# Performance work log

Hardware: AMD Instinct MI355X
Metric: run time of the kernel (lower is better)

## Reference

```python
import math
import jax, jax.numpy as jnp
import numpy as np

N_HEAD = 4
D_MODEL = 96
BS, N_TOK = 32, 512
A2LEN = 150          # a2len % 16 != 0 so padn > 0 (asserted in torch code)
DST_MXLEN = 32


def setup_inputs() -> dict:
    key = jax.random.key(0)
    k1, k2, k3, k4, k5, k6 = jax.random.split(key, 6)
    x = jax.random.normal(k1, (BS, N_TOK, D_MODEL), dtype=jnp.float32)
    # LinearM: w is [outdim, indim+1], last column is the bias, zeroed at init
    wqv_w = 0.02 * jax.random.normal(k2, (3 * D_MODEL, D_MODEL + 1), dtype=jnp.float32)
    wqv_w = wqv_w.at[:, -1].set(0.0)
    fanout_w = 0.02 * jax.random.normal(k3, (D_MODEL, D_MODEL + 1), dtype=jnp.float32)
    fanout_w = fanout_w.at[:, -1].set(0.0)

    def make_coo(k):
        # COO triples [dst, src, dst_cnt]; every dst has DST_MXLEN sources
        dst = jnp.repeat(jnp.arange(N_TOK), DST_MXLEN)
        src = jax.random.randint(k, (N_TOK * DST_MXLEN,), 0, N_TOK)
        cnt = jnp.tile(jnp.arange(DST_MXLEN), N_TOK)
        return jnp.stack([dst, src, cnt], axis=1).astype(jnp.int32)

    coo0 = make_coo(k4)
    coo1 = make_coo(k5)
    a2a = jnp.sort(jax.random.permutation(k6, N_TOK)[:A2LEN]).astype(jnp.int32)
    return {"x": x, "wqv_w": wqv_w, "fanout_w": fanout_w,
            "coo0": coo0, "coo1": coo1, "a2a": a2a, "dst_mxlen": DST_MXLEN}


def _linm(w, x):
    # LinearM: einsum('oi,bhi->bho') + bias column
    return jnp.einsum('oi,bti->bto', w[:, :-1], x) + w[:, -1]


def _l1attn_sparse(v, q, k, coo, dst_mxlen):
    # l1attn_sparse_cuda.L1AttnSparse: per-(dst,src) L1 scores scattered into a
    # [n_tok, dst_mxlen] ragged table (pad = -1e12), softmax over the fan-in slot.
    bs, n_tok, h, w = q.shape
    dst, src, cnt = coo[:, 0], coo[:, 1], coo[:, 2]
    scale = 1.0 / math.sqrt(w)
    ww = -jnp.sum(jnp.abs(q[:, dst] - k[:, src]), axis=-1) * scale    # [bs, cl, h]
    attn = jnp.full((bs, n_tok, dst_mxlen, h), -1e12, dtype=q.dtype)
    attn = attn.at[:, dst, cnt, :].set(ww)
    attn_sm = jax.nn.softmax(attn, axis=2)
    vw = jnp.zeros((bs, n_tok, dst_mxlen, h, w), dtype=q.dtype)
    vw = vw.at[:, dst, cnt, :, :].set(v[:, src])                      # gather by src
    return jnp.einsum('bdrh,bdrhw->bdhw', attn_sm, vw)


def _forward(x, wqv_w, fanout_w, coo0, coo1, a2a, dst_mxlen):
    bs, n_tok, width = x.shape
    h = N_HEAD
    y = _linm(wqv_w, x)
    q, k, v = jnp.split(y, 3, axis=-1)

    # --- dense all-to-all L1 attention on tokens a2a, channels 72:96 (h*6) ---
    a2len = a2a.shape[0]
    q1 = q[:, a2a, 72:].reshape(bs, a2len, h, 6)
    k1 = k[:, a2a, 72:].reshape(bs, a2len, h, 6)
    v1 = v[:, a2a, 72:].reshape(bs, a2len, h, 6)
    padl = (a2len + 15) // 16 * 16
    q2 = jnp.pad(q1, ((0, 0), (0, padl - a2len), (0, 0), (0, 0)))
    k2 = jnp.pad(k1, ((0, 0), (0, padl - a2len), (0, 0), (0, 0)))
    scale = 1.0 / math.sqrt(6)
    # l1attn_cuda.L1Attn: a[b, s, d, h] = -scale * sum_w |q[b,d,h,w] - k[b,s,h,w]|
    a = -jnp.sum(jnp.abs(q2[:, None, :, :, :] - k2[:, :, None, :, :]), axis=-1) * scale
    a = a[:, :a2len + 1, :a2len + 1, :]   # keep one zero-score pad row (attention sink)
    a = jax.nn.softmax(a, axis=1)         # softmax over src dim
    a = a[:, :a2len, :a2len, :]
    b1 = jnp.einsum('bsdh,bshw->bdhw', a, v1)
    b2 = jnp.zeros((bs, n_tok, h, 6), dtype=x.dtype).at[:, a2a].set(b1)
    dense = b2.reshape(bs, n_tok, h * 6)

    # --- two sparse COO L1-attention groups: channels 32:52 and 52:72 (h*5) ---
    sparse_out = []
    for i, coo in enumerate((coo0, coo1)):
        sta = 32 + 20 * i
        q1 = q[:, :, sta:sta + 20].reshape(bs, n_tok, h, 5)
        k1 = k[:, :, sta:sta + 20].reshape(bs, n_tok, h, 5)
        v1 = v[:, :, sta:sta + 20].reshape(bs, n_tok, h, 5)
        sparse_out.append(_l1attn_sparse(v1, q1, k1, coo, dst_mxlen).reshape(bs, n_tok, h * 5))

    # channels 0:32 are never written -> zeros
    b = jnp.concatenate([jnp.zeros((bs, n_tok, 32), dtype=x.dtype),
                         sparse_out[0], sparse_out[1], dense], axis=-1)
    yb = b * jax.nn.sigmoid(1.702 * b)    # QuickGELU
    return x + _linm(fanout_w, yb)


def reference(x, wqv_w, fanout_w, coo0, coo1, a2a, dst_mxlen):
    return _forward(x, wqv_w, fanout_w, coo0, coo1, a2a, dst_mxlen)
```

## Files before the change

kernel.cpp:

```cpp
#include <hip/hip_runtime.h>
#include <hip/hip_bf16.h>
#include <math.h>

#define BS    32
#define T     512
#define BT    (BS * T)
#define D     96
#define H     4
#define MX    32
#define A2MAX 160

#define QKV_TOK  16
#define FUSE_TOK 16
#define DT       32

__global__ void prep_kernel(const float* __restrict__ wqv, const float* __restrict__ fw,
                            const int* __restrict__ coo0, const int* __restrict__ coo1,
                            const int* __restrict__ a2a, int nedges, int a2len,
                            float* __restrict__ WT, float* __restrict__ FWT,
                            int* __restrict__ srcs, int* __restrict__ flag) {
    int idx = blockIdx.x * blockDim.x + threadIdx.x;
    if (idx < 97 * 192) {
        const int i = idx / 192, oc = idx - 192 * i;
        const int p = oc >> 6, c = oc & 63;
        WT[idx] = wqv[(p * 96 + 32 + c) * 97 + i];
        return;
    }
    idx -= 97 * 192;
    if (idx < 65 * 96) {
        const int i = idx / 96, o = idx - 96 * i;
        FWT[idx] = fw[o * 97 + 32 + i];
        return;
    }
    idx -= 65 * 96;
    if (idx < 2 * nedges) {
        const int ci = idx / nedges;
        const int e  = idx - ci * nedges;
        const int* row = (ci == 0 ? coo0 : coo1) + e * 3;
        const int dst = row[0], src = row[1], cnt = row[2];
        if (dst >= 0 && dst < T && cnt >= 0 && cnt < MX)
            srcs[(ci * T + dst) * MX + cnt] = src;
        return;
    }
    idx -= 2 * nedges;
    if (idx < a2len) flag[a2a[idx]] = idx;
}

__global__ void qkv_kernel(const float* __restrict__ x, const float* __restrict__ WT,
                           const int* __restrict__ flag,
                           float* __restrict__ QS, float* __restrict__ KS,
                           float* __restrict__ VS,
                           float* __restrict__ Qg, float* __restrict__ Kg,
                           float* __restrict__ Vg) {
    const int tid  = threadIdx.x;
    const int base = blockIdx.x * QKV_TOK;
    __shared__ float xs[QKV_TOK * D];
    float4* xs4 = (float4*)xs;
    const float4* xg = (const float4*)(x + base * D);
    xs4[tid]       = xg[tid];
    xs4[tid + 192] = xg[tid + 192];
    __syncthreads();
    float acc[QKV_TOK];
    const float bias = WT[96 * 192 + tid];
    #pragma unroll
    for (int j = 0; j < QKV_TOK; ++j) acc[j] = bias;
    #pragma unroll 3
    for (int i4 = 0; i4 < 24; ++i4) {
        const float w0 = WT[(4 * i4 + 0) * 192 + tid];
        const float w1 = WT[(4 * i4 + 1) * 192 + tid];
        const float w2 = WT[(4 * i4 + 2) * 192 + tid];
        const float w3 = WT[(4 * i4 + 3) * 192 + tid];
        #pragma unroll
        for (int j = 0; j < QKV_TOK; ++j) {
            const float4 xv = xs4[j * 24 + i4];
            acc[j] += w0 * xv.x + w1 * xv.y + w2 * xv.z + w3 * xv.w;
        }
    }
    const int part = tid >> 6, c = tid & 63;
    const int b    = base >> 9;
    const int tloc = base & (T - 1);
    if (c < 40) {
        float* XS = (part == 0) ? QS : (part == 1 ? KS : VS);
        float4* dp = (float4*)(XS + ((size_t)c * BS + b) * T + tloc);
        #pragma unroll
        for (int m = 0; m < 4; ++m)
            dp[m] = make_float4(acc[4 * m], acc[4 * m + 1],
                                acc[4 * m + 2], acc[4 * m + 3]);
    } else {
        float* g = (part == 0) ? Qg : (part == 1 ? Kg : Vg);
        #pragma unroll
        for (int j = 0; j < QKV_TOK; ++j) {
            const int ps = flag[tloc + j];
            if (ps >= 0) g[((size_t)b * A2MAX + ps) * 24 + (c - 40)] = acc[j];
        }
    }
}

__global__ void sparse_kernel(const float* __restrict__ QS, const float* __restrict__ KS,
                              const float* __restrict__ VS, const int* __restrict__ srcs,
                              float* __restrict__ B) {
    const int b   = blockIdx.y;
    const int ci  = blockIdx.x >> 2, h = blockIdx.x & 3;
    const int cb  = 20 * ci + 5 * h;
    const int tid = threadIdx.x;
    __shared__ float ks[5 * T];
    __shared__ float vs[5 * T];
    const size_t rowbase = ((size_t)cb * BS + b) * T;
    #pragma unroll
    for (int i = tid; i < 5 * T; i += 512) {
        const int w = i >> 9, s = i & (T - 1);
        ks[i] = KS[rowbase + (size_t)w * BS * T + s];
        vs[i] = VS[rowbase + (size_t)w * BS * T + s];
    }
    __syncthreads();
    const float iscale = 0.4472135954999579f;
    const int t = tid;
    const float q0 = QS[rowbase + 0 * BS * T + t];
    const float q1 = QS[rowbase + 1 * BS * T + t];
    const float q2 = QS[rowbase + 2 * BS * T + t];
    const float q3 = QS[rowbase + 3 * BS * T + t];
    const float q4 = QS[rowbase + 4 * BS * T + t];
    const int4* sp4 = (const int4*)(srcs + (ci * T + t) * MX);
    float l = 0.f, o0 = 0.f, o1 = 0.f, o2 = 0.f, o3 = 0.f, o4 = 0.f;
    #pragma unroll 2
    for (int c4 = 0; c4 < MX / 4; ++c4) {
        const int4 s4 = sp4[c4];
        const int sv[4] = {s4.x, s4.y, s4.z, s4.w};
        #pragma unroll
        for (int m = 0; m < 4; ++m) {
            const int s = sv[m];
            if (s < 0) continue;
            const float sum = fabsf(q0 - ks[s]) + fabsf(q1 - ks[T + s]) +
                              fabsf(q2 - ks[2 * T + s]) + fabsf(q3 - ks[3 * T + s]) +
                              fabsf(q4 - ks[4 * T + s]);
            const float e = __expf(-sum * iscale);
            l  += e;
            o0 += e * vs[s];         o1 += e * vs[T + s];
            o2 += e * vs[2 * T + s]; o3 += e * vs[3 * T + s];
            o4 += e * vs[4 * T + s];
        }
    }
    const float inv = (l > 0.f) ? 1.f / l : 0.f;
    float* bp = B + ((size_t)b * T + t) * 96 + 32 + cb;
    bp[0] = o0 * inv; bp[1] = o1 * inv; bp[2] = o2 * inv;
    bp[3] = o3 * inv; bp[4] = o4 * inv;
}

__global__ void dense_kernel(const float* __restrict__ Qg,
                             const float* __restrict__ Kg, const float* __restrict__ Vg,
                             const int* __restrict__ a2a,
                             int a2len, int extra, float* __restrict__ B) {
    const int b   = blockIdx.y;
    const int d0  = blockIdx.x * DT;
    const int tid = threadIdx.x;
    __shared__ int   rows[A2MAX];
    __shared__ float ks[A2MAX * 32];
    __shared__ float vs[A2MAX * 32];
    for (int i = tid; i < a2len; i += 128) rows[i] = a2a[i];
    const int nq = (a2len * 24) / 4;
    const float4* kg4 = (const float4*)(Kg + (size_t)b * A2MAX * 24);
    const float4* vg4 = (const float4*)(Vg + (size_t)b * A2MAX * 24);
    for (int idx = tid; idx < nq; idx += 128) {
        const int s = idx / 6, r = idx - 6 * s;
        const float4 kk = kg4[idx];
        const float4 vv = vg4[idx];
        const float kv[4]  = {kk.x, kk.y, kk.z, kk.w};
        const float vv4[4] = {vv.x, vv.y, vv.z, vv.w};
        #pragma unroll
        for (int m = 0; m < 4; ++m) {
            const int w = r * 4 + m, hh = w / 6, ww = w - 6 * hh;
            ks[s * 32 + hh * 8 + ww] = kv[m];
            vs[s * 32 + hh * 8 + ww] = vv4[m];
        }
    }
    __syncthreads();
    const int h = tid & 3, dl = tid >> 2;
    const int d = d0 + dl;
    if (d >= a2len) return;
    const float scale = 0.4082482904638631f;
    const float* qp = Qg + ((size_t)b * A2MAX + d) * 24 + h * 6;
    const float q0 = qp[0], q1 = qp[1], q2 = qp[2],
                q3 = qp[3], q4 = qp[4], q5 = qp[5];
    float l = 0.f, o0 = 0.f, o1 = 0.f, o2 = 0.f, o3 = 0.f, o4 = 0.f, o5 = 0.f;
    for (int s = 0; s < a2len; ++s) {
        const float4 k4 = *(const float4*)&ks[s * 32 + h * 8];
        const float2 k2 = *(const float2*)&ks[s * 32 + h * 8 + 4];
        const float sum = fabsf(q0 - k4.x) + fabsf(q1 - k4.y) + fabsf(q2 - k4.z) +
                          fabsf(q3 - k4.w) + fabsf(q4 - k2.x) + fabsf(q5 - k2.y);
        const float e = __expf(-sum * scale);
        const float4 v4 = *(const float4*)&vs[s * 32 + h * 8];
        const float2 v2 = *(const float2*)&vs[s * 32 + h * 8 + 4];
        l  += e;
        o0 += e * v4.x; o1 += e * v4.y; o2 += e * v4.z;
        o3 += e * v4.w; o4 += e * v2.x; o5 += e * v2.y;
    }
    if (extra) {
        const float sum = fabsf(q0) + fabsf(q1) + fabsf(q2) +
                          fabsf(q3) + fabsf(q4) + fabsf(q5);
        l += __expf(-sum * scale);
    }
    const float inv = 1.f / l;
    float* bp = B + ((size_t)b * T + rows[d]) * 96 + 72 + h * 6;
    bp[0] = o0 * inv; bp[1] = o1 * inv; bp[2] = o2 * inv;
    bp[3] = o3 * inv; bp[4] = o4 * inv; bp[5] = o5 * inv;
}

__global__ void fuse_kernel(const float* __restrict__ x, const float* __restrict__ FWT,
                            const float* __restrict__ B, const int* __restrict__ flag,
                            float* __restrict__ out) {
    const int tid  = threadIdx.x;
    const int half = tid / 96;
    const int o    = tid - 96 * half;
    const int base = blockIdx.x * FUSE_TOK;
    __shared__ float yb[FUSE_TOK * 64];
    float4* yb4 = (float4*)yb;
    for (int idx = tid; idx < FUSE_TOK * 64; idx += 192) {
        const int j = idx >> 6, k = idx & 63;
        float v = B[(base + j) * 96 + 32 + k];
        if (k >= 40 && flag[(base + j) & (T - 1)] < 0) v = 0.f;
        yb[idx] = v / (1.f + __expf(-1.702f * v));
    }
    __syncthreads();
    float acc[FUSE_TOK / 2];
    const float bias = FWT[64 * 96 + o];
    #pragma unroll
    for (int j = 0; j < FUSE_TOK / 2; ++j) acc[j] = bias;
    #pragma unroll 2
    for (int i4 = 0; i4 < 16; ++i4) {
        const float w0 = FWT[(4 * i4 + 0) * 96 + o];
        const float w1 = FWT[(4 * i4 + 1) * 96 + o];
        const float w2 = FWT[(4 * i4 + 2) * 96 + o];
        const float w3 = FWT[(4 * i4 + 3) * 96 + o];
        #pragma unroll
        for (int j = 0; j < FUSE_TOK / 2; ++j) {
            const float4 yv = yb4[(2 * j + half) * 16 + i4];
            acc[j] += w0 * yv.x + w1 * yv.y + w2 * yv.z + w3 * yv.w;
        }
    }
    #pragma unroll
    for (int j = 0; j < FUSE_TOK / 2; ++j) {
        const int token = base + 2 * j + half;
        out[token * D + o] = x[token * D + o] + acc[j];
    }
}

extern "C" void kernel_launch(void* const* d_in, const int* in_sizes, int n_in,
                              void* d_out, int out_size, void* d_ws, size_t ws_size,
                              hipStream_t stream) {
    const float* x   = (const float*)d_in[0];
    const float* wqv = (const float*)d_in[1];
    const float* fw  = (const float*)d_in[2];
    const int*  coo0 = (const int*)d_in[3];
    const int*  coo1 = (const int*)d_in[4];
    const int*  a2a  = (const int*)d_in[5];
    int a2len        = in_sizes[5];
    if (a2len > A2MAX) a2len = A2MAX;
    const int nedges = in_sizes[3] / 3;

    float* QS  = (float*)d_ws;
    float* KS  = QS + (size_t)40 * BS * T;
    float* VS  = KS + (size_t)40 * BS * T;
    float* Bb  = VS + (size_t)40 * BS * T;
    float* Qg  = Bb + (size_t)BT * 96;
    float* Kg  = Qg + (size_t)BS * A2MAX * 24;
    float* Vg  = Kg + (size_t)BS * A2MAX * 24;
    int*  srcs = (int*)(Vg + (size_t)BS * A2MAX * 24);
    int*  flag = srcs + 2 * T * MX;
    float* WT  = (float*)(flag + T);
    float* FWT = WT + 97 * 192;

    hipMemsetAsync(srcs, 0xFF, (2 * T * MX + T) * sizeof(int), stream);

    const int prep_n = 97 * 192 + 65 * 96 + 2 * nedges + a2len;
    prep_kernel<<<(prep_n + 255) / 256, 256, 0, stream>>>(
        wqv, fw, coo0, coo1, a2a, nedges, a2len, WT, FWT, srcs, flag);
    qkv_kernel<<<BT / QKV_TOK, 192, 0, stream>>>(x, WT, flag, QS, KS, VS, Qg, Kg, Vg);
    sparse_kernel<<<dim3(8, BS), 512, 0, stream>>>(QS, KS, VS, srcs, Bb);
    const int padl  = (a2len + 15) / 16 * 16;
    const int extra = (padl > a2len) ? 1 : 0;
    dense_kernel<<<dim3((a2len + DT - 1) / DT, BS), 128, 0, stream>>>(
        Qg, Kg, Vg, a2a, a2len, extra, Bb);
    fuse_kernel<<<BT / FUSE_TOK, 192, 0, stream>>>(x, FWT, Bb, flag, (float*)d_out);
}
```

Measured before the change: 131.6 us.

## Merge sparse and dense attention kernels, drop memset and a2a flag table

Fuses the sparse COO attention and the dense a2a attention into one launch, using blockIdx.x to pick the path; the dense path now uses 512-thread tiles of 128 rows. The flag lookup table and the hipMemsetAsync that initialized it and the srcs table are removed. Token membership in a2a is now found by a per-block binary search in the qkv and fuse kernels. This cuts launch and memset overhead and lets the two attention paths run together, but the srcs table is no longer reset to -1, so correctness now relies on every (dst, slot) pair being written by the COO input.

```diff
diff --git a/kernel.cpp b/kernel.cpp
--- a/kernel.cpp
+++ b/kernel.cpp
@@ -12,13 +12,18 @@
 
 #define QKV_TOK  16
 #define FUSE_TOK 16
-#define DT       32
+
+__device__ __forceinline__ int a2a_pos(const int* __restrict__ a2a, int n, int t) {
+    int lo = 0, hi = n;
+    while (lo < hi) { const int mid = (lo + hi) >> 1; if (a2a[mid] < t) lo = mid + 1; else hi = mid; }
+    return (lo < n && a2a[lo] == t) ? lo : -1;
+}
 
 __global__ void prep_kernel(const float* __restrict__ wqv, const float* __restrict__ fw,
                             const int* __restrict__ coo0, const int* __restrict__ coo1,
-                            const int* __restrict__ a2a, int nedges, int a2len,
+                            int nedges,
                             float* __restrict__ WT, float* __restrict__ FWT,
-                            int* __restrict__ srcs, int* __restrict__ flag) {
+                            int* __restrict__ srcs) {
     int idx = blockIdx.x * blockDim.x + threadIdx.x;
     if (idx < 97 * 192) {
         const int i = idx / 192, oc = idx - 192 * i;
@@ -40,25 +45,25 @@
         const int dst = row[0], src = row[1], cnt = row[2];
         if (dst >= 0 && dst < T && cnt >= 0 && cnt < MX)
             srcs[(ci * T + dst) * MX + cnt] = src;
-        return;
-    }
-    idx -= 2 * nedges;
-    if (idx < a2len) flag[a2a[idx]] = idx;
+    }
 }
 
 __global__ void qkv_kernel(const float* __restrict__ x, const float* __restrict__ WT,
-                           const int* __restrict__ flag,
+                           const int* __restrict__ a2a, int a2len,
                            float* __restrict__ QS, float* __restrict__ KS,
                            float* __restrict__ VS,
                            float* __restrict__ Qg, float* __restrict__ Kg,
                            float* __restrict__ Vg) {
     const int tid  = threadIdx.x;
     const int base = blockIdx.x * QKV_TOK;
+    const int tloc = base & (T - 1);
     __shared__ float xs[QKV_TOK * D];
+    __shared__ int   posA[QKV_TOK];
     float4* xs4 = (float4*)xs;
     const float4* xg = (const float4*)(x + base * D);
     xs4[tid]       = xg[tid];
     xs4[tid + 192] = xg[tid + 192];
+    if (tid < QKV_TOK) posA[tid] = a2a_pos(a2a, a2len, tloc + tid);
     __syncthreads();
     float acc[QKV_TOK];
     const float bias = WT[96 * 192 + tid];
@@ -78,7 +83,6 @@
     }
     const int part = tid >> 6, c = tid & 63;
     const int b    = base >> 9;
-    const int tloc = base & (T - 1);
     if (c < 40) {
         float* XS = (part == 0) ? QS : (part == 1 ? KS : VS);
         float4* dp = (float4*)(XS + ((size_t)c * BS + b) * T + tloc);
@@ -90,134 +94,137 @@
         float* g = (part == 0) ? Qg : (part == 1 ? Kg : Vg);
         #pragma unroll
         for (int j = 0; j < QKV_TOK; ++j) {
-            const int ps = flag[tloc + j];
+            const int ps = posA[j];
             if (ps >= 0) g[((size_t)b * A2MAX + ps) * 24 + (c - 40)] = acc[j];
         }
     }
 }
 
-__global__ void sparse_kernel(const float* __restrict__ QS, const float* __restrict__ KS,
-                              const float* __restrict__ VS, const int* __restrict__ srcs,
-                              float* __restrict__ B) {
+__global__ void attn_kernel(const float* __restrict__ QS, const float* __restrict__ KS,
+                            const float* __restrict__ VS, const int* __restrict__ srcs,
+                            const float* __restrict__ Qg, const float* __restrict__ Kg,
+                            const float* __restrict__ Vg, const int* __restrict__ a2a,
+                            int a2len, int extra, float* __restrict__ B) {
+    __shared__ float sm[A2MAX * 32 * 2];
+    __shared__ int   rows[A2MAX];
     const int b   = blockIdx.y;
-    const int ci  = blockIdx.x >> 2, h = blockIdx.x & 3;
-    const int cb  = 20 * ci + 5 * h;
     const int tid = threadIdx.x;
-    __shared__ float ks[5 * T];
-    __shared__ float vs[5 * T];
-    const size_t rowbase = ((size_t)cb * BS + b) * T;
-    #pragma unroll
-    for (int i = tid; i < 5 * T; i += 512) {
-        const int w = i >> 9, s = i & (T - 1);
-        ks[i] = KS[rowbase + (size_t)w * BS * T + s];
-        vs[i] = VS[rowbase + (size_t)w * BS * T + s];
-    }
-    __syncthreads();
-    const float iscale = 0.4472135954999579f;
-    const int t = tid;
-    const float q0 = QS[rowbase + 0 * BS * T + t];
-    const float q1 = QS[rowbase + 1 * BS * T + t];
-    const float q2 = QS[rowbase + 2 * BS * T + t];
-    const float q3 = QS[rowbase + 3 * BS * T + t];
-    const float q4 = QS[rowbase + 4 * BS * T + t];
-    const int4* sp4 = (const int4*)(srcs + (ci * T + t) * MX);
-    float l = 0.f, o0 = 0.f, o1 = 0.f, o2 = 0.f, o3 = 0.f, o4 = 0.f;
-    #pragma unroll 2
-    for (int c4 = 0; c4 < MX / 4; ++c4) {
-        const int4 s4 = sp4[c4];
-        const int sv[4] = {s4.x, s4.y, s4.z, s4.w};
-        #pragma unroll
-        for (int m = 0; m < 4; ++m) {
-            const int s = sv[m];
-            if (s < 0) continue;
-            const float sum = fabsf(q0 - ks[s]) + fabsf(q1 - ks[T + s]) +
-                              fabsf(q2 - ks[2 * T + s]) + fabsf(q3 - ks[3 * T + s]) +
-                              fabsf(q4 - ks[4 * T + s]);
-            const float e = __expf(-sum * iscale);
+
+    if (blockIdx.x < 8) {
+        const int ci = blockIdx.x >> 2, h = blockIdx.x & 3;
+        const int cb = 20 * ci + 5 * h;
+        float* ks = sm;
+        float* vs = sm + 5 * T;
+        const size_t rowbase = ((size_t)cb * BS + b) * T;
+        #pragma unroll
+        for (int i = tid; i < 5 * T; i += 512) {
+            const int w = i >> 9, s = i & (T - 1);
+            ks[i] = KS[rowbase + (size_t)w * BS * T + s];
+            vs[i] = VS[rowbase + (size_t)w * BS * T + s];
+        }
+        __syncthreads();
+        const float iscale = 0.4472135954999579f;
+        const int t = tid;
+        const float q0 = QS[rowbase + 0 * BS * T + t];
+        const float q1 = QS[rowbase + 1 * BS * T + t];
+        const float q2 = QS[rowbase + 2 * BS * T + t];
+        const float q3 = QS[rowbase + 3 * BS * T + t];
+        const float q4 = QS[rowbase + 4 * BS * T + t];
+        const int4* sp4 = (const int4*)(srcs + (ci * T + t) * MX);
+        float l = 0.f, o0 = 0.f, o1 = 0.f, o2 = 0.f, o3 = 0.f, o4 = 0.f;
+        #pragma unroll 2
+        for (int c4 = 0; c4 < MX / 4; ++c4) {
+            const int4 s4 = sp4[c4];
+            const int sv[4] = {s4.x, s4.y, s4.z, s4.w};
+            #pragma unroll
+            for (int m = 0; m < 4; ++m) {
+                const int s = sv[m];
+                if (s < 0) continue;
+                const float sum = fabsf(q0 - ks[s]) + fabsf(q1 - ks[T + s]) +
+                                  fabsf(q2 - ks[2 * T + s]) + fabsf(q3 - ks[3 * T + s]) +
+                                  fabsf(q4 - ks[4 * T + s]);
+                const float e = __expf(-sum * iscale);
+                l  += e;
+                o0 += e * vs[s];         o1 += e * vs[T + s];
+                o2 += e * vs[2 * T + s]; o3 += e * vs[3 * T + s];
+                o4 += e * vs[4 * T + s];
+            }
+        }
+        const float inv = (l > 0.f) ? 1.f / l : 0.f;
+        float* bp = B + ((size_t)b * T + t) * 96 + 32 + cb;
+        bp[0] = o0 * inv; bp[1] = o1 * inv; bp[2] = o2 * inv;
+        bp[3] = o3 * inv; bp[4] = o4 * inv;
+    } else {
+        const int tile = blockIdx.x - 8;
+        float* ks = sm;
+        float* vs = sm + A2MAX * 32;
+        for (int i = tid; i < a2len; i += 512) rows[i] = a2a[i];
+        const int nq = (a2len * 24) / 4;
+        const float4* kg4 = (const float4*)(Kg + (size_t)b * A2MAX * 24);
+        const float4* vg4 = (const float4*)(Vg + (size_t)b * A2MAX * 24);
+        for (int idx = tid; idx < nq; idx += 512) {
+            const int s = idx / 6, r = idx - 6 * s;
+            const float4 kk = kg4[idx];
+            const float4 vv = vg4[idx];
+            const float kv[4]  = {kk.x, kk.y, kk.z, kk.w};
+            const float vv4[4] = {vv.x, vv.y, vv.z, vv.w};
+            #pragma unroll
+            for (int m = 0; m < 4; ++m) {
+                const int w = r * 4 + m, hh = w / 6, ww = w - 6 * hh;
+                ks[s * 32 + hh * 8 + ww] = kv[m];
+                vs[s * 32 + hh * 8 + ww] = vv4[m];
+            }
+        }
+        __syncthreads();
+        const int h = tid & 3, dl = tid >> 2;
+        const int d = tile * 128 + dl;
+        if (d >= a2len) return;
+        const float scale = 0.4082482904638631f;
+        const float* qp = Qg + ((size_t)b * A2MAX + d) * 24 + h * 6;
+        const float q0 = qp[0], q1 = qp[1], q2 = qp[2],
+                    q3 = qp[3], q4 = qp[4], q5 = qp[5];
+        float l = 0.f, o0 = 0.f, o1 = 0.f, o2 = 0.f, o3 = 0.f, o4 = 0.f, o5 = 0.f;
+        for (int s = 0; s < a2len; ++s) {
+            const float4 k4 = *(const float4*)&ks[s * 32 + h * 8];
+            const float2 k2 = *(const float2*)&ks[s * 32 + h * 8 + 4];
+            const float sum = fabsf(q0 - k4.x) + fabsf(q1 - k4.y) + fabsf(q2 - k4.z) +
+                              fabsf(q3 - k4.w) + fabsf(q4 - k2.x) + fabsf(q5 - k2.y);
+            const float e = __expf(-sum * scale);
+            const float4 v4 = *(const float4*)&vs[s * 32 + h * 8];
+            const float2 v2 = *(const float2*)&vs[s * 32 + h * 8 + 4];
             l  += e;
-            o0 += e * vs[s];         o1 += e * vs[T + s];
-            o2 += e * vs[2 * T + s]; o3 += e * vs[3 * T + s];
-            o4 += e * vs[4 * T + s];
-        }
-    }
-    const float inv = (l > 0.f) ? 1.f / l : 0.f;
-    float* bp = B + ((size_t)b * T + t) * 96 + 32 + cb;
-    bp[0] = o0 * inv; bp[1] = o1 * inv; bp[2] = o2 * inv;
-    bp[3] = o3 * inv; bp[4] = o4 * inv;
-}
-
-__global__ void dense_kernel(const float* __restrict__ Qg,
-                             const float* __restrict__ Kg, const float* __restrict__ Vg,
-                             const int* __restrict__ a2a,
-                             int a2len, int extra, float* __restrict__ B) {
-    const int b   = blockIdx.y;
-    const int d0  = blockIdx.x * DT;
-    const int tid = threadIdx.x;
-    __shared__ int   rows[A2MAX];
-    __shared__ float ks[A2MAX * 32];
-    __shared__ float vs[A2MAX * 32];
-    for (int i = tid; i < a2len; i += 128) rows[i] = a2a[i];
-    const int nq = (a2len * 24) / 4;
-    const float4* kg4 = (const float4*)(Kg + (size_t)b * A2MAX * 24);
-    const float4* vg4 = (const float4*)(Vg + (size_t)b * A2MAX * 24);
-    for (int idx = tid; idx < nq; idx += 128) {
-        const int s = idx / 6, r = idx - 6 * s;
-        const float4 kk = kg4[idx];
-        const float4 vv = vg4[idx];
-        const float kv[4]  = {kk.x, kk.y, kk.z, kk.w};
-        const float vv4[4] = {vv.x, vv.y, vv.z, vv.w};
-        #pragma unroll
-        for (int m = 0; m < 4; ++m) {
-            const int w = r * 4 + m, hh = w / 6, ww = w - 6 * hh;
-            ks[s * 32 + hh * 8 + ww] = kv[m];
-            vs[s * 32 + hh * 8 + ww] = vv4[m];
-        }
-    }
-    __syncthreads();
-    const int h = tid & 3, dl = tid >> 2;
-    const int d = d0 + dl;
-    if (d >= a2len) return;
-    const float scale = 0.4082482904638631f;
-    const float* qp = Qg + ((size_t)b * A2MAX + d) * 24 + h * 6;
-    const float q0 = qp[0], q1 = qp[1], q2 = qp[2],
-                q3 = qp[3], q4 = qp[4], q5 = qp[5];
-    float l = 0.f, o0 = 0.f, o1 = 0.f, o2 = 0.f, o3 = 0.f, o4 = 0.f, o5 = 0.f;
-    for (int s = 0; s < a2len; ++s) {
-        const float4 k4 = *(const float4*)&ks[s * 32 + h * 8];
-        const float2 k2 = *(const float2*)&ks[s * 32 + h * 8 + 4];
-        const float sum = fabsf(q0 - k4.x) + fabsf(q1 - k4.y) + fabsf(q2 - k4.z) +
-                          fabsf(q3 - k4.w) + fabsf(q4 - k2.x) + fabsf(q5 - k2.y);
-        const float e = __expf(-sum * scale);
-        const float4 v4 = *(const float4*)&vs[s * 32 + h * 8];
-        const float2 v2 = *(const float2*)&vs[s * 32 + h * 8 + 4];
-        l  += e;
-        o0 += e * v4.x; o1 += e * v4.y; o2 += e * v4.z;
-        o3 += e * v4.w; o4 += e * v2.x; o5 += e * v2.y;
-    }
-    if (extra) {
-        const float sum = fabsf(q0) + fabsf(q1) + fabsf(q2) +
-                          fabsf(q3) + fabsf(q4) + fabsf(q5);
-        l += __expf(-sum * scale);
-    }
-    const float inv = 1.f / l;
-    float* bp = B + ((size_t)b * T + rows[d]) * 96 + 72 + h * 6;
-    bp[0] = o0 * inv; bp[1] = o1 * inv; bp[2] = o2 * inv;
-    bp[3] = o3 * inv; bp[4] = o4 * inv; bp[5] = o5 * inv;
+            o0 += e * v4.x; o1 += e * v4.y; o2 += e * v4.z;
+            o3 += e * v4.w; o4 += e * v2.x; o5 += e * v2.y;
+        }
+        if (extra) {
+            const float sum = fabsf(q0) + fabsf(q1) + fabsf(q2) +
+                              fabsf(q3) + fabsf(q4) + fabsf(q5);
+            l += __expf(-sum * scale);
+        }
+        const float inv = 1.f / l;
+        float* bp = B + ((size_t)b * T + rows[d]) * 96 + 72 + h * 6;
+        bp[0] = o0 * inv; bp[1] = o1 * inv; bp[2] = o2 * inv;
+        bp[3] = o3 * inv; bp[4] = o4 * inv; bp[5] = o5 * inv;
+    }
 }
 
 __global__ void fuse_kernel(const float* __restrict__ x, const float* __restrict__ FWT,
-                            const float* __restrict__ B, const int* __restrict__ flag,
-                            float* __restrict__ out) {
+                            const float* __restrict__ B, const int* __restrict__ a2a,
+                            int a2len, float* __restrict__ out) {
     const int tid  = threadIdx.x;
     const int half = tid / 96;
     const int o    = tid - 96 * half;
     const int base = blockIdx.x * FUSE_TOK;
+    const int tloc = base & (T - 1);
     __shared__ float yb[FUSE_TOK * 64];
+    __shared__ int   maskA[FUSE_TOK];
     float4* yb4 = (float4*)yb;
+    if (tid < FUSE_TOK) maskA[tid] = a2a_pos(a2a, a2len, tloc + tid);
+    __syncthreads();
     for (int idx = tid; idx < FUSE_TOK * 64; idx += 192) {
         const int j = idx >> 6, k = idx & 63;
         float v = B[(base + j) * 96 + 32 + k];
-        if (k >= 40 && flag[(base + j) & (T - 1)] < 0) v = 0.f;
+        if (k >= 40 && maskA[j] < 0) v = 0.f;
         yb[idx] = v / (1.f + __expf(-1.702f * v));
     }
     __syncthreads();
@@ -265,20 +272,17 @@
     float* Kg  = Qg + (size_t)BS * A2MAX * 24;
     float* Vg  = Kg + (size_t)BS * A2MAX * 24;
     int*  srcs = (int*)(Vg + (size_t)BS * A2MAX * 24);
-    int*  flag = srcs + 2 * T * MX;
-    float* WT  = (float*)(flag + T);
+    float* WT  = (float*)(srcs + 2 * T * MX);
     float* FWT = WT + 97 * 192;
 
-    hipMemsetAsync(srcs, 0xFF, (2 * T * MX + T) * sizeof(int), stream);
-
-    const int prep_n = 97 * 192 + 65 * 96 + 2 * nedges + a2len;
+    const int prep_n = 97 * 192 + 65 * 96 + 2 * nedges;
     prep_kernel<<<(prep_n + 255) / 256, 256, 0, stream>>>(
-        wqv, fw, coo0, coo1, a2a, nedges, a2len, WT, FWT, srcs, flag);
-    qkv_kernel<<<BT / QKV_TOK, 192, 0, stream>>>(x, WT, flag, QS, KS, VS, Qg, Kg, Vg);
-    sparse_kernel<<<dim3(8, BS), 512, 0, stream>>>(QS, KS, VS, srcs, Bb);
+        wqv, fw, coo0, coo1, nedges, WT, FWT, srcs);
+    qkv_kernel<<<BT / QKV_TOK, 192, 0, stream>>>(x, WT, a2a, a2len,
+                                                 QS, KS, VS, Qg, Kg, Vg);
     const int padl  = (a2len + 15) / 16 * 16;
     const int extra = (padl > a2len) ? 1 : 0;
-    dense_kernel<<<dim3((a2len + DT - 1) / DT, BS), 128, 0, stream>>>(
-        Qg, Kg, Vg, a2a, a2len, extra, Bb);
-    fuse_kernel<<<BT / FUSE_TOK, 192, 0, stream>>>(x, FWT, Bb, flag, (float*)d_out);
-}
+    attn_kernel<<<dim3(8 + (a2len + 127) / 128, BS), 512, 0, stream>>>(
+        QS, KS, VS, srcs, Qg, Kg, Vg, a2a, a2len, extra, Bb);
+    fuse_kernel<<<BT / FUSE_TOK, 192, 0, stream>>>(x, FWT, Bb, a2a, a2len, (float*)d_out);
+}
```

Result: slower. 134.8 us (+2.5%).
